# Kernel optimization log

Hardware: AMD Instinct MI355X
Metric: run time of the kernel (lower is better)

Reference implementation:

```python
import jax, jax.numpy as jnp
import numpy as np

K = 1  # top-k experts per image


def cv_squared(v):
    # squared coefficient of variation; torch .var() is unbiased -> ddof=1
    eps = 1e-10
    m = v.mean()
    var = v.var(ddof=1)
    return jnp.where(jnp.abs(m) < eps, jnp.zeros((), v.dtype), var / (m * m + eps))


def setup_inputs() -> dict:
    key = jax.random.key(0)
    k0, k1, k2, k3 = jax.random.split(key, 4)
    B, H, W, C, E, HID = 64, 32, 32, 512, 5, 2048
    x = jax.random.normal(k0, (B, H, W, C), jnp.float32)
    # xavier-uniform-like scale for the gate
    gate_scale = float(np.sqrt(6.0 / (C + E)))
    w_gate = jax.random.uniform(k1, (C, E), jnp.float32, -gate_scale, gate_scale)
    W1 = jax.random.normal(k2, (E, C, HID), jnp.float32) * 0.02
    b1 = jnp.zeros((E, HID), jnp.float32)
    W2 = jax.random.normal(k3, (E, HID, C), jnp.float32) * 0.02
    b2 = jnp.zeros((E, C), jnp.float32)
    return {"x": x, "w_gate": w_gate, "W1": W1, "b1": b1, "W2": W2, "b2": b2}


def reference(x, w_gate, W1, b1, W2, b2):
    B, H, W_, C = x.shape
    E = w_gate.shape[1]
    xt = x.reshape(B, H * W_, C)              # [B, T, C] tokens
    xg = x.mean(axis=(1, 2))                  # [B, C] per-image gating feature

    # eval-mode noisy_top_k_gating (no noise): clean logits, clamp, top-k softmax
    logits = jnp.clip(xg @ w_gate, -50.0, 50.0)          # [B, E]
    top_logits, top_idx = jax.lax.top_k(logits, min(K + 1, E))
    tk_logits = top_logits[:, :K]
    tk_idx = top_idx[:, :K]                               # [B, K]
    tk_gates = jax.nn.softmax(tk_logits, axis=1)          # [B, K]
    gates = jnp.zeros_like(logits).at[jnp.arange(B)[:, None], tk_idx].set(tk_gates)

    importance = gates.sum(axis=0)                        # [E]
    load = (gates > 0).sum(axis=0).astype(jnp.float32)    # [E]
    loss = jnp.clip(cv_squared(importance) + cv_squared(load), 0.0, 1000.0)

    # dispatch: every token of image b goes through its top-K experts
    y = jnp.zeros_like(xt)
    for ki in range(K):
        idx = tk_idx[:, ki]                               # [B] expert id per image
        h = jnp.einsum('btd,bdh->bth', xt, W1[idx]) + b1[idx][:, None, :]
        h = jax.nn.gelu(h, approximate=False)             # torch nn.GELU default (erf)
        o = jnp.einsum('bth,bhd->btd', h, W2[idx]) + b2[idx][:, None, :]
        y = y + tk_gates[:, ki][:, None, None] * o

    return y.reshape(B, H, W_, C), loss
```

## Files before the change

### kernel.cpp

```cpp
#include <hip/hip_runtime.h>
#include <hip/hip_bf16.h>
#include <math.h>

typedef __attribute__((ext_vector_type(4))) float f4_t;
typedef __attribute__((ext_vector_type(8))) short s8_t;

constexpr int Bc = 64;
constexpr int Tc = 1024;
constexpr int Cc = 512;
constexpr int Ec = 5;
constexpr int HIDc = 2048;

__device__ __forceinline__ void async_copy16(const void* gsrc, void* ldst) {
  __builtin_amdgcn_global_load_lds(
      (const __attribute__((address_space(1))) unsigned int*)gsrc,
      (__attribute__((address_space(3))) unsigned int*)ldst, 16, 0, 0);
}

__device__ __forceinline__ float gelu_f(float v) {
  float v2 = v * v;
  float z = v * (1.5957691216f + 0.0713548162f * v2);
  float e = __expf(z);
  float r = __frcp_rn(1.0f + e);
  return v - v * r;
}


__global__ void k_prep(const float* __restrict__ x, ushort* __restrict__ xbf,
                       float* __restrict__ part) {
  int b = blockIdx.x, p = blockIdx.y, tid = threadIdx.x;
  const float4* xp = (const float4*)(x + ((size_t)b * Tc + (size_t)p * 128) * Cc);
  ushort4* op = (ushort4*)(xbf + ((size_t)b * Tc + (size_t)p * 128) * Cc);
  int c4 = tid & 127, r0 = tid >> 7;
  float4 s = {0.f, 0.f, 0.f, 0.f};
  for (int r = r0; r < 128; r += 2) {
    float4 v = xp[(size_t)r * 128 + c4];
    s.x += v.x; s.y += v.y; s.z += v.z; s.w += v.w;
    union { __hip_bfloat16 h[4]; ushort4 u; } cv;
    cv.h[0] = __float2bfloat16(v.x);
    cv.h[1] = __float2bfloat16(v.y);
    cv.h[2] = __float2bfloat16(v.z);
    cv.h[3] = __float2bfloat16(v.w);
    op[(size_t)r * 128 + c4] = cv.u;
  }
  __shared__ float4 sh[128];
  if (r0) sh[c4] = s;
  __syncthreads();
  if (!r0) {
    float4 o = sh[c4];
    s.x += o.x; s.y += o.y; s.z += o.z; s.w += o.w;
    ((float4*)part)[(size_t)(b * 8 + p) * 128 + c4] = s;
  }
}

__global__ void k_partial(const float* __restrict__ x, float* __restrict__ part) {
  int b = blockIdx.x, p = blockIdx.y, tid = threadIdx.x;
  const float* xp = x + ((size_t)b * Tc + (size_t)p * 128) * Cc;
  float s0 = 0.f, s1 = 0.f;
  for (int t = 0; t < 128; ++t) {
    s0 += xp[(size_t)t * Cc + tid];
    s1 += xp[(size_t)t * Cc + tid + 256];
  }
  part[(size_t)(b * 8 + p) * Cc + tid] = s0;
  part[(size_t)(b * 8 + p) * Cc + tid + 256] = s1;
}

__global__ void k_cvt_x(const float* __restrict__ src, ushort* __restrict__ dst, int n4) {
  int i = blockIdx.x * blockDim.x + threadIdx.x;
  int stride = gridDim.x * blockDim.x;
  const float4* s4 = (const float4*)src;
  ushort4* d4 = (ushort4*)dst;
  for (; i < n4; i += stride) {
    float4 v = s4[i];
    union { __hip_bfloat16 h[4]; ushort4 u; } cv;
    cv.h[0] = __float2bfloat16(v.x);
    cv.h[1] = __float2bfloat16(v.y);
    cv.h[2] = __float2bfloat16(v.z);
    cv.h[3] = __float2bfloat16(v.w);
    d4[i] = cv.u;
  }
}

__global__ void k_xg_logits(const float* __restrict__ part, const float* __restrict__ wg,
                            float* __restrict__ logits) {
  __shared__ float xg[Cc];
  __shared__ float red[Ec][4];
  int b = blockIdx.x, tid = threadIdx.x;
  for (int c = tid; c < Cc; c += 256) {
    float s = 0.f;
#pragma unroll
    for (int p = 0; p < 8; ++p) s += part[(size_t)(b * 8 + p) * Cc + c];
    xg[c] = s * (1.0f / 1024.0f);
  }
  __syncthreads();
  float le[Ec] = {0.f, 0.f, 0.f, 0.f, 0.f};
  for (int c = tid; c < Cc; c += 256) {
    float v = xg[c];
#pragma unroll
    for (int e = 0; e < Ec; ++e) le[e] += v * wg[c * Ec + e];
  }
#pragma unroll
  for (int e = 0; e < Ec; ++e) {
    float v = le[e];
#pragma unroll
    for (int off = 32; off > 0; off >>= 1) v += __shfl_down(v, off);
    if ((tid & 63) == 0) red[e][tid >> 6] = v;
  }
  __syncthreads();
  if (tid < Ec) {
    float v = red[tid][0] + red[tid][1] + red[tid][2] + red[tid][3];
    v = fminf(fmaxf(v, -50.f), 50.f);
    logits[b * Ec + tid] = v;
  }
}

__global__ void k_gate(const float* __restrict__ logits, int* __restrict__ idx,
                       float* __restrict__ loss_out) {
  __shared__ int cnt[Ec];
  int tid = threadIdx.x;
  if (tid < Ec) cnt[tid] = 0;
  __syncthreads();
  if (tid < Bc) {
    const float* lb = logits + tid * Ec;
    int best = 0;
    float bv = lb[0];
#pragma unroll
    for (int e = 1; e < Ec; ++e) {
      float v = lb[e];
      if (v > bv) { bv = v; best = e; }
    }
    idx[tid] = best;
    atomicAdd(&cnt[best], 1);
  }
  __syncthreads();
  if (tid == 0) {
    const float mean = (float)Bc / (float)Ec;
    float var = 0.f;
#pragma unroll
    for (int e = 0; e < Ec; ++e) {
      float d = (float)cnt[e] - mean;
      var += d * d;
    }
    var *= (1.0f / (Ec - 1));
    float loss = 2.f * (var / (mean * mean + 1e-10f));
    loss = fminf(fmaxf(loss, 0.f), 1000.f);
    *loss_out = loss;
  }
}

__global__ void k_transpose_cvt(const float* __restrict__ src, __hip_bfloat16* __restrict__ dst,
                                int K, int N) {
  __shared__ float tile[32][33];
  int e = blockIdx.z;
  int kb = blockIdx.y * 32, nb = blockIdx.x * 32;
  const float* s = src + (size_t)e * K * N;
  __hip_bfloat16* d = dst + (size_t)e * K * N;
  int lx = threadIdx.x & 31, ly = threadIdx.x >> 5;
#pragma unroll
  for (int r = 0; r < 4; ++r) {
    int k = kb + ly + r * 8;
    tile[ly + r * 8][lx] = s[(size_t)k * N + nb + lx];
  }
  __syncthreads();
#pragma unroll
  for (int r = 0; r < 4; ++r) {
    int n = nb + ly + r * 8;
    d[(size_t)n * K + kb + lx] = __float2bfloat16(tile[lx][ly + r * 8]);
  }
}


#define GEMM_PRELUDE(KDIM)                                               \
  int tid = threadIdx.x, l = tid & 63, w = tid >> 6;                     \
  int wr = w >> 2, wc = w & 3;                                           \
  const short* gA[4];                                                    \
  const short* gB[4];                                                    \
  int loff[4];                                                           \
  _Pragma("unroll")                                                      \
  for (int i = 0; i < 4; ++i) {                                          \
    int sp = i * 512 + tid;                                              \
    int r = sp >> 3;                                                     \
    int c8 = ((sp & 7) ^ (r & 7)) << 3;                                  \
    gA[i] = Ab + (size_t)r * (KDIM) + c8;                                \
    gB[i] = Bb + (size_t)r * (KDIM) + c8;                                \
    loff[i] = sp * 16;                                                   \
  }                                                                      \
  int abase = (wr * 128 + (l & 15)) * 128;                               \
  int bbase = (wc * 64 + (l & 15)) * 128;                                \
  int s0 = (((l >> 4)) ^ (l & 7)) << 4;                                  \
  int s1 = (((l >> 4) + 4) ^ (l & 7)) << 4;

#define STAGE_A_HALF(buf, h, kt)                                         \
  {                                                                      \
    char* d_ = (char*)&lds[buf][0][0];                                   \
    int k0_ = (kt) * 64;                                                 \
    async_copy16(gA[2 * (h)] + k0_, d_ + loff[2 * (h)]);                 \
    async_copy16(gA[2 * (h) + 1] + k0_, d_ + loff[2 * (h) + 1]);         \
  }
#define STAGE_B_HALF(buf, h, kt)                                         \
  {                                                                      \
    char* d_ = (char*)&lds[buf][1][0];                                   \
    int k0_ = (kt) * 64;                                                 \
    async_copy16(gB[2 * (h)] + k0_, d_ + loff[2 * (h)]);                 \
    async_copy16(gB[2 * (h) + 1] + k0_, d_ + loff[2 * (h) + 1]);         \
  }

#define READ_QUAD(AFR, bufp, qq)                                         \
  {                                                                      \
    const char* Aq_ = (const char*)&lds[bufp][0][0];                     \
    AFR[0] = *(const s8_t*)(Aq_ + abase + ((qq) * 2 + 0) * 2048 + s0);   \
    AFR[1] = *(const s8_t*)(Aq_ + abase + ((qq) * 2 + 0) * 2048 + s1);   \
    AFR[2] = *(const s8_t*)(Aq_ + abase + ((qq) * 2 + 1) * 2048 + s0);   \
    AFR[3] = *(const s8_t*)(Aq_ + abase + ((qq) * 2 + 1) * 2048 + s1);   \
  }

#define READ_BFR(bufp)                                                   \
  {                                                                      \
    const char* Bq_ = (const char*)&lds[bufp][1][0];                     \
    _Pragma("unroll")                                                    \
    for (int fn = 0; fn < 4; ++fn) {                                     \
      bfr[fn * 2 + 0] = *(const s8_t*)(Bq_ + bbase + fn * 2048 + s0);    \
      bfr[fn * 2 + 1] = *(const s8_t*)(Bq_ + bbase + fn * 2048 + s1);    \
    }                                                                    \
  }

#define BAR()                          \
  __builtin_amdgcn_s_barrier();        \
  asm volatile("" ::: "memory")

#define MFMA_CLUSTER(q, AFR)                                                 \
  __builtin_amdgcn_s_setprio(1);                                             \
  _Pragma("unroll")                                                          \
  for (int kk = 0; kk < 2; ++kk)                                             \
    _Pragma("unroll")                                                        \
    for (int j = 0; j < 2; ++j)                                              \
      _Pragma("unroll")                                                      \
      for (int fn = 0; fn < 4; ++fn)                                         \
        acc[(q) * 2 + j][fn] = __builtin_amdgcn_mfma_f32_16x16x32_bf16(      \
            AFR[j * 2 + kk], bfr[fn * 2 + kk], acc[(q) * 2 + j][fn], 0, 0, 0); \
  __builtin_amdgcn_s_setprio(0);

#define TILE4(tt, NTv)                                                   \
  {                                                                      \
    const int cb_ = (tt) & 1;                                            \
                            \
    if ((tt) + 1 < (NTv)) STAGE_A_HALF(cb_ ^ 1, 0, (tt) + 1)             \
    READ_BFR(cb_)                                                        \
    READ_QUAD(afrA, cb_, 0)                                              \
    MFMA_CLUSTER(0, afrA)                                                \
    READ_QUAD(afrB, cb_, 1)                                              \
    BAR();                                                               \
                                                                 \
    MFMA_CLUSTER(1, afrB)                                                \
    if ((tt) + 1 < (NTv)) STAGE_A_HALF(cb_ ^ 1, 1, (tt) + 1)             \
    READ_QUAD(afrA, cb_, 2)                                              \
    BAR();                                                               \
                                                                 \
    MFMA_CLUSTER(2, afrA)                                                \
    if ((tt) + 2 < (NTv)) STAGE_B_HALF(cb_, 0, (tt) + 2)                 \
    READ_QUAD(afrB, cb_, 3)                                              \
    BAR();                                                               \
                                                                 \
    MFMA_CLUSTER(3, afrB)                                                \
    if ((tt) + 2 < (NTv)) {                                              \
      STAGE_B_HALF(cb_, 1, (tt) + 2)                                     \
      asm volatile("s_waitcnt vmcnt(4)" ::: "memory");                   \
    } else if ((tt) + 1 < (NTv)) {                                       \
      asm volatile("s_waitcnt vmcnt(0)" ::: "memory");                   \
    }                                                                    \
    BAR();                                                               \
  }

#define KLOOP_P(NTv)                                                     \
  s8_t bfr[8], afrA[4], afrB[4];                                         \
  STAGE_B_HALF(0, 0, 0)                                                  \
  STAGE_B_HALF(0, 1, 0)                                                  \
  STAGE_A_HALF(0, 0, 0)                                                  \
  STAGE_A_HALF(0, 1, 0)                                                  \
  STAGE_B_HALF(1, 0, 1)                                                  \
  STAGE_B_HALF(1, 1, 1)                                                  \
  asm volatile("s_waitcnt vmcnt(4)" ::: "memory");                       \
  BAR();                                                                 \
  _Pragma("unroll 2")                                                    \
  for (int t = 0; t < (NTv); ++t) {                                      \
    TILE4(t, NTv)                                                        \
  }

__global__ __launch_bounds__(512, 2) void k_gemm1(
    const __hip_bfloat16* __restrict__ xbf, const __hip_bfloat16* __restrict__ w1t,
    const float* __restrict__ b1, const int* __restrict__ idx, int b0, int nz,
    __hip_bfloat16* __restrict__ h) {
  constexpr int K = Cc;
  constexpr int N = HIDc;
  constexpr int NT = K / 64;
  constexpr int NBX = N / 256, NBY = Tc / 256;
  __shared__ short lds[2][2][256 * 64];

  int nwg = NBX * NBY * nz;
  int cpx = nwg >> 3;
  int lg = (blockIdx.x & 7) * cpx + (blockIdx.x >> 3);
  int bx = lg % NBX, by = (lg / NBX) % NBY, bz = lg / (NBX * NBY);

  int e = idx[b0 + bz];
  int m0 = by * 256, n0 = bx * 256;
  const short* Ab = (const short*)xbf + ((size_t)bz * Tc + m0) * K;
  const short* Bb = (const short*)w1t + ((size_t)e * N + n0) * K;

  GEMM_PRELUDE(K)
  f4_t acc[8][4] = {};
  { KLOOP_P(NT) }

  __syncthreads();
  short* chunk = &lds[0][0][0] + w * (64 * 72);
  const float* bias = b1 + (size_t)e * N;
  short* hb = (short*)(h + (size_t)bz * Tc * N);
  int cc2 = (l & 7) * 8;
#pragma unroll
  for (int p = 0; p < 2; ++p) {
#pragma unroll
    for (int fn = 0; fn < 4; ++fn) {
      float bv = bias[n0 + wc * 64 + fn * 16 + (l & 15)];
#pragma unroll
      for (int fm = 0; fm < 4; ++fm) {
        int rl = fm * 16 + ((l >> 4) << 2);
#pragma unroll
        for (int j = 0; j < 4; ++j) {
          float v = gelu_f(acc[p * 4 + fm][fn][j] + bv);
          chunk[(rl + j) * 72 + fn * 16 + (l & 15)] =
              (short)__bfloat16_as_ushort(__float2bfloat16(v));
        }
      }
    }
#pragma unroll
    for (int q = 0; q < 8; ++q) {
      int rr = q * 8 + (l >> 3);
      s8_t v = *(const s8_t*)(chunk + rr * 72 + cc2);
      *(s8_t*)(hb + (size_t)(m0 + wr * 128 + p * 64 + rr) * N + n0 + wc * 64 + cc2) = v;
    }
    asm volatile("s_waitcnt lgkmcnt(0)" ::: "memory");
  }
}

__global__ __launch_bounds__(512, 2) void k_gemm2(
    const __hip_bfloat16* __restrict__ h, const __hip_bfloat16* __restrict__ w2t,
    const float* __restrict__ b2, const int* __restrict__ idx, int b0, int nz,
    float* __restrict__ out) {
  constexpr int K = HIDc;
  constexpr int N = Cc;
  constexpr int NT = K / 64;
  constexpr int NBX = N / 256, NBY = Tc / 256;
  __shared__ short lds[2][2][256 * 64];

  int nwg = NBX * NBY * nz;
  int cpx = nwg >> 3;
  int lg = (blockIdx.x & 7) * cpx + (blockIdx.x >> 3);
  int bx = lg % NBX, by = (lg / NBX) % NBY, bz = lg / (NBX * NBY);

  int e = idx[b0 + bz];
  int m0 = by * 256, n0 = bx * 256;
  const short* Ab = (const short*)h + ((size_t)bz * Tc + m0) * K;
  const short* Bb = (const short*)w2t + ((size_t)e * N + n0) * K;

  GEMM_PRELUDE(K)
  f4_t acc[8][4] = {};
  { KLOOP_P(NT) }

  float* ob = out + (size_t)(b0 + bz) * Tc * N;
  const float* bias = b2 + (size_t)e * N;
#pragma unroll
  for (int fn = 0; fn < 4; ++fn) {
    int col = n0 + wc * 64 + fn * 16 + (l & 15);
    float bv = bias[col];
#pragma unroll
    for (int fm = 0; fm < 8; ++fm) {
      int rbase = m0 + wr * 128 + fm * 16 + ((l >> 4) << 2);
#pragma unroll
      for (int j = 0; j < 4; ++j) {
        ob[(size_t)(rbase + j) * N + col] = acc[fm][fn][j] + bv;
      }
    }
  }
}

extern "C" void kernel_launch(void* const* d_in, const int* in_sizes, int n_in,
                              void* d_out, int out_size, void* d_ws, size_t ws_size,
                              hipStream_t stream) {
  const float* x  = (const float*)d_in[0];
  const float* wg = (const float*)d_in[1];
  const float* W1 = (const float*)d_in[2];
  const float* b1 = (const float*)d_in[3];
  const float* W2 = (const float*)d_in[4];
  const float* b2 = (const float*)d_in[5];
  float* out = (float*)d_out;

  char* ws = (char*)d_ws;
  size_t off = 0;
  float* part = (float*)(ws + off); off += (size_t)Bc * 8 * Cc * 4;
  float* logits = (float*)(ws + off); off += (size_t)Bc * Ec * 4;
  int* idx = (int*)(ws + off); off += (size_t)Bc * 4;
  off = (off + 255) & ~(size_t)255;
  __hip_bfloat16* w1t = (__hip_bfloat16*)(ws + off); off += (size_t)Ec * HIDc * Cc * 2;
  __hip_bfloat16* w2t = (__hip_bfloat16*)(ws + off); off += (size_t)Ec * HIDc * Cc * 2;
  size_t dynoff = (off + 255) & ~(size_t)255;

  const size_t x_all = (size_t)Bc * Tc * Cc * 2;
  const size_t x_per_b = (size_t)Tc * Cc * 2;
  const size_t h_per_b = (size_t)Tc * HIDc * 2;

  k_transpose_cvt<<<dim3(HIDc / 32, Cc / 32, Ec), 256, 0, stream>>>(W1, w1t, Cc, HIDc);
  k_transpose_cvt<<<dim3(Cc / 32, HIDc / 32, Ec), 256, 0, stream>>>(W2, w2t, HIDc, Cc);

  if (ws_size >= dynoff + x_all + h_per_b) {
    __hip_bfloat16* xbf = (__hip_bfloat16*)(ws + dynoff);
    __hip_bfloat16* hbf = (__hip_bfloat16*)(ws + dynoff + x_all);
    int cb = (int)((ws_size - dynoff - x_all) / h_per_b);
    if (cb > Bc) cb = Bc;

    k_prep<<<dim3(Bc, 8), 256, 0, stream>>>(x, (ushort*)xbf, part);
    k_xg_logits<<<dim3(Bc), 256, 0, stream>>>(part, wg, logits);
    k_gate<<<dim3(1), 256, 0, stream>>>(logits, idx, out + ((size_t)out_size - 1));

    for (int b0 = 0; b0 < Bc; b0 += cb) {
      int c = (Bc - b0) < cb ? (Bc - b0) : cb;
      const __hip_bfloat16* xc = xbf + (size_t)b0 * Tc * Cc;
      k_gemm1<<<dim3((HIDc / 256) * (Tc / 256) * c), 512, 0, stream>>>(
          xc, w1t, b1, idx, b0, c, hbf);
      k_gemm2<<<dim3((Cc / 256) * (Tc / 256) * c), 512, 0, stream>>>(
          hbf, w2t, b2, idx, b0, c, out);
    }
  } else {
    size_t avail = ws_size > dynoff ? ws_size - dynoff : 0;
    int cb = (int)(avail / (x_per_b + h_per_b));
    if (cb > Bc) cb = Bc;
    if (cb < 1) cb = 1;
    __hip_bfloat16* xbf = (__hip_bfloat16*)(ws + dynoff);
    __hip_bfloat16* hbf = (__hip_bfloat16*)(ws + dynoff + (size_t)cb * x_per_b);

    k_partial<<<dim3(Bc, 8), 256, 0, stream>>>(x, part);
    k_xg_logits<<<dim3(Bc), 256, 0, stream>>>(part, wg, logits);
    k_gate<<<dim3(1), 256, 0, stream>>>(logits, idx, out + ((size_t)out_size - 1));

    for (int b0 = 0; b0 < Bc; b0 += cb) {
      int c = (Bc - b0) < cb ? (Bc - b0) : cb;
      int n4 = c * (Tc * Cc / 4);
      k_cvt_x<<<dim3(1024), 256, 0, stream>>>(x + (size_t)b0 * Tc * Cc, (ushort*)xbf, n4);
      k_gemm1<<<dim3((HIDc / 256) * (Tc / 256) * c), 512, 0, stream>>>(
          xbf, w1t, b1, idx, b0, c, hbf);
      k_gemm2<<<dim3((Cc / 256) * (Tc / 256) * c), 512, 0, stream>>>(
          hbf, w2t, b2, idx, b0, c, out);
    }
  }
}
```

Measured before the change: 436.5 us.

## Process two N-tiles per workgroup in both expert GEMMs to reuse A loads

Each workgroup in gemm1 now covers two 256-wide N tiles (512 columns), and each in gemm2 covers the full 512 output columns. The K-loop runs straight through both tiles, emitting the first tile's epilogue mid-loop before resetting the accumulators. This halves the number of workgroups and lets the pipelined prefetch continue across tiles, cutting per-block prologue and epilogue cost and improving locality on the shared A rows. The gemm1 epilogue now goes through a small dedicated LDS scratch buffer, and the XCD remap handles workgroup counts that do not divide by 8. The trade-off is fewer workgroups, so less parallelism for the GPU to spread across its compute units, plus extra LDS use.

```diff
diff --git a/kernel.cpp b/kernel.cpp
--- a/kernel.cpp
+++ b/kernel.cpp
@@ -190,19 +190,17 @@
   int s0 = (((l >> 4)) ^ (l & 7)) << 4;                                  \
   int s1 = (((l >> 4) + 4) ^ (l & 7)) << 4;
 
-#define STAGE_A_HALF(buf, h, kt)                                         \
+#define STAGE_A_HALF(buf, h, off)                                        \
   {                                                                      \
     char* d_ = (char*)&lds[buf][0][0];                                   \
-    int k0_ = (kt) * 64;                                                 \
-    async_copy16(gA[2 * (h)] + k0_, d_ + loff[2 * (h)]);                 \
-    async_copy16(gA[2 * (h) + 1] + k0_, d_ + loff[2 * (h) + 1]);         \
-  }
-#define STAGE_B_HALF(buf, h, kt)                                         \
+    async_copy16(gA[2 * (h)] + (off), d_ + loff[2 * (h)]);               \
+    async_copy16(gA[2 * (h) + 1] + (off), d_ + loff[2 * (h) + 1]);       \
+  }
+#define STAGE_B_HALF(buf, h, off)                                        \
   {                                                                      \
     char* d_ = (char*)&lds[buf][1][0];                                   \
-    int k0_ = (kt) * 64;                                                 \
-    async_copy16(gB[2 * (h)] + k0_, d_ + loff[2 * (h)]);                 \
-    async_copy16(gB[2 * (h) + 1] + k0_, d_ + loff[2 * (h) + 1]);         \
+    async_copy16(gB[2 * (h)] + (off), d_ + loff[2 * (h)]);               \
+    async_copy16(gB[2 * (h) + 1] + (off), d_ + loff[2 * (h) + 1]);       \
   }
 
 #define READ_QUAD(AFR, bufp, qq)                                         \
@@ -240,11 +238,11 @@
             AFR[j * 2 + kk], bfr[fn * 2 + kk], acc[(q) * 2 + j][fn], 0, 0, 0); \
   __builtin_amdgcn_s_setprio(0);
 
-#define TILE4(tt, NTv)                                                   \
+#define TILE4(tt, NTv, aoff1, boff2)                                     \
   {                                                                      \
     const int cb_ = (tt) & 1;                                            \
                             \
-    if ((tt) + 1 < (NTv)) STAGE_A_HALF(cb_ ^ 1, 0, (tt) + 1)             \
+    if ((tt) + 1 < (NTv)) STAGE_A_HALF(cb_ ^ 1, 0, aoff1)                \
     READ_BFR(cb_)                                                        \
     READ_QUAD(afrA, cb_, 0)                                              \
     MFMA_CLUSTER(0, afrA)                                                \
@@ -252,18 +250,18 @@
     BAR();                                                               \
                                                                  \
     MFMA_CLUSTER(1, afrB)                                                \
-    if ((tt) + 1 < (NTv)) STAGE_A_HALF(cb_ ^ 1, 1, (tt) + 1)             \
+    if ((tt) + 1 < (NTv)) STAGE_A_HALF(cb_ ^ 1, 1, aoff1)                \
     READ_QUAD(afrA, cb_, 2)                                              \
     BAR();                                                               \
                                                                  \
     MFMA_CLUSTER(2, afrA)                                                \
-    if ((tt) + 2 < (NTv)) STAGE_B_HALF(cb_, 0, (tt) + 2)                 \
+    if ((tt) + 2 < (NTv)) STAGE_B_HALF(cb_, 0, boff2)                    \
     READ_QUAD(afrB, cb_, 3)                                              \
     BAR();                                                               \
                                                                  \
     MFMA_CLUSTER(3, afrB)                                                \
     if ((tt) + 2 < (NTv)) {                                              \
-      STAGE_B_HALF(cb_, 1, (tt) + 2)                                     \
+      STAGE_B_HALF(cb_, 1, boff2)                                        \
       asm volatile("s_waitcnt vmcnt(4)" ::: "memory");                   \
     } else if ((tt) + 1 < (NTv)) {                                       \
       asm volatile("s_waitcnt vmcnt(0)" ::: "memory");                   \
@@ -271,19 +269,44 @@
     BAR();                                                               \
   }
 
-#define KLOOP_P(NTv)                                                     \
-  s8_t bfr[8], afrA[4], afrB[4];                                         \
-  STAGE_B_HALF(0, 0, 0)                                                  \
-  STAGE_B_HALF(0, 1, 0)                                                  \
-  STAGE_A_HALF(0, 0, 0)                                                  \
-  STAGE_A_HALF(0, 1, 0)                                                  \
-  STAGE_B_HALF(1, 0, 1)                                                  \
-  STAGE_B_HALF(1, 1, 1)                                                  \
-  asm volatile("s_waitcnt vmcnt(4)" ::: "memory");                       \
-  BAR();                                                                 \
-  _Pragma("unroll 2")                                                    \
-  for (int t = 0; t < (NTv); ++t) {                                      \
-    TILE4(t, NTv)                                                        \
+#define ACC_RESET()                                                      \
+  _Pragma("unroll")                                                      \
+  for (int fm = 0; fm < 8; ++fm)                                         \
+    _Pragma("unroll")                                                    \
+    for (int fn = 0; fn < 4; ++fn) acc[fm][fn] = (f4_t){0.f, 0.f, 0.f, 0.f};
+
+#define EPILOGUE1(n0e)                                                   \
+  {                                                                      \
+    short* chunk = scr + w * (16 * 72);                                  \
+    int cc2 = (l & 7) * 8;                                               \
+    float bv4[4];                                                        \
+    _Pragma("unroll")                                                    \
+    for (int fn = 0; fn < 4; ++fn)                                       \
+      bv4[fn] = bias[(n0e) + wc * 64 + fn * 16 + (l & 15)];              \
+    _Pragma("unroll")                                                    \
+    for (int p = 0; p < 2; ++p) {                                        \
+      _Pragma("unroll")                                                  \
+      for (int fm = 0; fm < 4; ++fm) {                                   \
+        _Pragma("unroll")                                                \
+        for (int fn = 0; fn < 4; ++fn) {                                 \
+          _Pragma("unroll")                                              \
+          for (int j = 0; j < 4; ++j) {                                  \
+            float v = gelu_f(acc[p * 4 + fm][fn][j] + bv4[fn]);          \
+            chunk[(((l >> 4) << 2) + j) * 72 + fn * 16 + (l & 15)] =     \
+                (short)__bfloat16_as_ushort(__float2bfloat16(v));        \
+          }                                                              \
+        }                                                                \
+        asm volatile("s_waitcnt lgkmcnt(0)" ::: "memory");               \
+        _Pragma("unroll")                                                \
+        for (int q = 0; q < 2; ++q) {                                    \
+          int rr = q * 8 + (l >> 3);                                     \
+          s8_t v = *(const s8_t*)(chunk + rr * 72 + cc2);                \
+          *(s8_t*)(hb + (size_t)(m0 + wr * 128 + p * 64 + fm * 16 + rr) * HIDc + \
+                   (n0e) + wc * 64 + cc2) = v;                           \
+        }                                                                \
+        asm volatile("s_waitcnt lgkmcnt(0)" ::: "memory");               \
+      }                                                                  \
+    }                                                                    \
   }
 
 __global__ __launch_bounds__(512, 2) void k_gemm1(
@@ -291,54 +314,46 @@
     const float* __restrict__ b1, const int* __restrict__ idx, int b0, int nz,
     __hip_bfloat16* __restrict__ h) {
   constexpr int K = Cc;
-  constexpr int N = HIDc;
-  constexpr int NT = K / 64;
-  constexpr int NBX = N / 256, NBY = Tc / 256;
+  constexpr int NBX = HIDc / 512, NBY = Tc / 256;
   __shared__ short lds[2][2][256 * 64];
+  __shared__ short scr[8 * 16 * 72];
 
   int nwg = NBX * NBY * nz;
-  int cpx = nwg >> 3;
-  int lg = (blockIdx.x & 7) * cpx + (blockIdx.x >> 3);
+  int q_ = nwg >> 3, r_ = nwg & 7;
+  int xcd = blockIdx.x & 7, j_ = blockIdx.x >> 3;
+  int lg = (xcd < r_ ? xcd * (q_ + 1) : r_ * (q_ + 1) + (xcd - r_) * q_) + j_;
   int bx = lg % NBX, by = (lg / NBX) % NBY, bz = lg / (NBX * NBY);
 
   int e = idx[b0 + bz];
-  int m0 = by * 256, n0 = bx * 256;
+  int m0 = by * 256, n0 = bx * 512;
   const short* Ab = (const short*)xbf + ((size_t)bz * Tc + m0) * K;
-  const short* Bb = (const short*)w1t + ((size_t)e * N + n0) * K;
+  const short* Bb = (const short*)w1t + ((size_t)e * HIDc + n0) * K;
 
   GEMM_PRELUDE(K)
   f4_t acc[8][4] = {};
-  { KLOOP_P(NT) }
-
-  __syncthreads();
-  short* chunk = &lds[0][0][0] + w * (64 * 72);
-  const float* bias = b1 + (size_t)e * N;
-  short* hb = (short*)(h + (size_t)bz * Tc * N);
-  int cc2 = (l & 7) * 8;
-#pragma unroll
-  for (int p = 0; p < 2; ++p) {
-#pragma unroll
-    for (int fn = 0; fn < 4; ++fn) {
-      float bv = bias[n0 + wc * 64 + fn * 16 + (l & 15)];
-#pragma unroll
-      for (int fm = 0; fm < 4; ++fm) {
-        int rl = fm * 16 + ((l >> 4) << 2);
-#pragma unroll
-        for (int j = 0; j < 4; ++j) {
-          float v = gelu_f(acc[p * 4 + fm][fn][j] + bv);
-          chunk[(rl + j) * 72 + fn * 16 + (l & 15)] =
-              (short)__bfloat16_as_ushort(__float2bfloat16(v));
-        }
-      }
-    }
-#pragma unroll
-    for (int q = 0; q < 8; ++q) {
-      int rr = q * 8 + (l >> 3);
-      s8_t v = *(const s8_t*)(chunk + rr * 72 + cc2);
-      *(s8_t*)(hb + (size_t)(m0 + wr * 128 + p * 64 + rr) * N + n0 + wc * 64 + cc2) = v;
-    }
-    asm volatile("s_waitcnt lgkmcnt(0)" ::: "memory");
-  }
+  short* hb = (short*)(h + (size_t)bz * Tc * HIDc);
+  const float* bias = b1 + (size_t)e * HIDc;
+
+  s8_t bfr[8], afrA[4], afrB[4];
+  STAGE_B_HALF(0, 0, 0)
+  STAGE_B_HALF(0, 1, 0)
+  STAGE_A_HALF(0, 0, 0)
+  STAGE_A_HALF(0, 1, 0)
+  STAGE_B_HALF(1, 0, 64)
+  STAGE_B_HALF(1, 1, 64)
+  asm volatile("s_waitcnt vmcnt(4)" ::: "memory");
+  BAR();
+#pragma unroll 2
+  for (int t = 0; t < 16; ++t) {
+    int aoff1 = ((t + 1) & 7) * 64;
+    int boff2 = (((t + 2) >> 3) * 256) * K + ((t + 2) & 7) * 64;
+    TILE4(t, 16, aoff1, boff2)
+    if (t == 7) {
+      EPILOGUE1(n0)
+      ACC_RESET()
+    }
+  }
+  EPILOGUE1(n0 + 256)
 }
 
 __global__ __launch_bounds__(512, 2) void k_gemm2(
@@ -347,39 +362,60 @@
     float* __restrict__ out) {
   constexpr int K = HIDc;
   constexpr int N = Cc;
-  constexpr int NT = K / 64;
-  constexpr int NBX = N / 256, NBY = Tc / 256;
+  constexpr int NBY = Tc / 256;
   __shared__ short lds[2][2][256 * 64];
 
-  int nwg = NBX * NBY * nz;
-  int cpx = nwg >> 3;
-  int lg = (blockIdx.x & 7) * cpx + (blockIdx.x >> 3);
-  int bx = lg % NBX, by = (lg / NBX) % NBY, bz = lg / (NBX * NBY);
+  int nwg = NBY * nz;
+  int q_ = nwg >> 3, r_ = nwg & 7;
+  int xcd = blockIdx.x & 7, j_ = blockIdx.x >> 3;
+  int lg = (xcd < r_ ? xcd * (q_ + 1) : r_ * (q_ + 1) + (xcd - r_) * q_) + j_;
+  int by = lg % NBY, bz = lg / NBY;
 
   int e = idx[b0 + bz];
-  int m0 = by * 256, n0 = bx * 256;
+  int m0 = by * 256;
   const short* Ab = (const short*)h + ((size_t)bz * Tc + m0) * K;
-  const short* Bb = (const short*)w2t + ((size_t)e * N + n0) * K;
+  const short* Bb = (const short*)w2t + (size_t)e * N * K;
 
   GEMM_PRELUDE(K)
   f4_t acc[8][4] = {};
-  { KLOOP_P(NT) }
-
   float* ob = out + (size_t)(b0 + bz) * Tc * N;
   const float* bias = b2 + (size_t)e * N;
-#pragma unroll
-  for (int fn = 0; fn < 4; ++fn) {
-    int col = n0 + wc * 64 + fn * 16 + (l & 15);
-    float bv = bias[col];
-#pragma unroll
-    for (int fm = 0; fm < 8; ++fm) {
-      int rbase = m0 + wr * 128 + fm * 16 + ((l >> 4) << 2);
-#pragma unroll
-      for (int j = 0; j < 4; ++j) {
-        ob[(size_t)(rbase + j) * N + col] = acc[fm][fn][j] + bv;
-      }
-    }
-  }
+
+#define STORE2(n0e)                                                      \
+  _Pragma("unroll")                                                      \
+  for (int fn = 0; fn < 4; ++fn) {                                       \
+    int col = (n0e) + wc * 64 + fn * 16 + (l & 15);                      \
+    float bv = bias[col];                                                \
+    _Pragma("unroll")                                                    \
+    for (int fm = 0; fm < 8; ++fm) {                                     \
+      int rbase = m0 + wr * 128 + fm * 16 + ((l >> 4) << 2);             \
+      _Pragma("unroll")                                                  \
+      for (int j = 0; j < 4; ++j)                                        \
+        ob[(size_t)(rbase + j) * N + col] = acc[fm][fn][j] + bv;         \
+    }                                                                    \
+  }
+
+  s8_t bfr[8], afrA[4], afrB[4];
+  STAGE_B_HALF(0, 0, 0)
+  STAGE_B_HALF(0, 1, 0)
+  STAGE_A_HALF(0, 0, 0)
+  STAGE_A_HALF(0, 1, 0)
+  STAGE_B_HALF(1, 0, 64)
+  STAGE_B_HALF(1, 1, 64)
+  asm volatile("s_waitcnt vmcnt(4)" ::: "memory");
+  BAR();
+#pragma unroll 2
+  for (int t = 0; t < 64; ++t) {
+    int aoff1 = ((t + 1) & 31) * 64;
+    int boff2 = (((t + 2) >> 5) * 256) * K + ((t + 2) & 31) * 64;
+    TILE4(t, 64, aoff1, boff2)
+    if (t == 31) {
+      STORE2(0)
+      ACC_RESET()
+    }
+  }
+  STORE2(256)
+#undef STORE2
 }
 
 extern "C" void kernel_launch(void* const* d_in, const int* in_sizes, int n_in,
@@ -423,9 +459,9 @@
     for (int b0 = 0; b0 < Bc; b0 += cb) {
       int c = (Bc - b0) < cb ? (Bc - b0) : cb;
       const __hip_bfloat16* xc = xbf + (size_t)b0 * Tc * Cc;
-      k_gemm1<<<dim3((HIDc / 256) * (Tc / 256) * c), 512, 0, stream>>>(
+      k_gemm1<<<dim3((HIDc / 512) * (Tc / 256) * c), 512, 0, stream>>>(
           xc, w1t, b1, idx, b0, c, hbf);
-      k_gemm2<<<dim3((Cc / 256) * (Tc / 256) * c), 512, 0, stream>>>(
+      k_gemm2<<<dim3((Tc / 256) * c), 512, 0, stream>>>(
           hbf, w2t, b2, idx, b0, c, out);
     }
   } else {
@@ -444,9 +480,9 @@
       int c = (Bc - b0) < cb ? (Bc - b0) : cb;
       int n4 = c * (Tc * Cc / 4);
       k_cvt_x<<<dim3(1024), 256, 0, stream>>>(x + (size_t)b0 * Tc * Cc, (ushort*)xbf, n4);
-      k_gemm1<<<dim3((HIDc / 256) * (Tc / 256) * c), 512, 0, stream>>>(
+      k_gemm1<<<dim3((HIDc / 512) * (Tc / 256) * c), 512, 0, stream>>>(
           xbf, w1t, b1, idx, b0, c, hbf);
-      k_gemm2<<<dim3((Cc / 256) * (Tc / 256) * c), 512, 0, stream>>>(
+      k_gemm2<<<dim3((Tc / 256) * c), 512, 0, stream>>>(
           hbf, w2t, b2, idx, b0, c, out);
     }
   }
```

After: 681.1 us. 56.0% more time.
